# Kernel tuning notes

Measured on AMD Instinct MI355X. Metric: run time of the kernel, lower is better.

The kernel has to match this reference:

```python
import jax, jax.numpy as jnp
import numpy as np

B, N, F_IN, C_OUT = 128, 512, 2, 64
C_IN = F_IN + C_OUT           # 66, concat(input, state) feature dim
MLP_IN = (2 * 3 + 1) * C_IN   # order=2, support_len=3 -> 462


def _gcn(x, supports, W, b):
    """Diffusion conv: x [B,N,F]; for each support a, 2 diffusion orders."""
    outs = [x]
    for a in supports:
        x1 = jnp.einsum('bnf,nm->bmf', x, a)
        x2 = jnp.einsum('bnf,nm->bmf', x1, a)
        outs += [x1, x2]
    h = jnp.concatenate(outs, axis=2)  # [B, N, 7*F]
    return h @ W + b                   # Linear (dropout is eval-mode identity)


def setup_inputs() -> dict:
    key = jax.random.key(0)
    ks = jax.random.split(key, 12)
    return {
        'input': jax.random.normal(ks[0], (B, N, F_IN), dtype=jnp.float32),
        'state': jax.random.normal(ks[1], (B, N, C_OUT), dtype=jnp.float32),
        'A0':    jax.random.uniform(ks[2], (N, N), dtype=jnp.float32),
        'A1':    jax.random.uniform(ks[3], (N, N), dtype=jnp.float32),
        'nv1_1': jax.random.normal(ks[4], (N, 10), dtype=jnp.float32),
        'nv2_1': jax.random.normal(ks[5], (10, N), dtype=jnp.float32),
        'W1':    jax.random.normal(ks[6], (MLP_IN, 2 * C_OUT), dtype=jnp.float32) * 0.02,
        'b1':    jnp.zeros((2 * C_OUT,), dtype=jnp.float32),
        'nv1_2': jax.random.normal(ks[7], (N, 10), dtype=jnp.float32),
        'nv2_2': jax.random.normal(ks[8], (10, N), dtype=jnp.float32),
        'W2':    jax.random.normal(ks[9], (MLP_IN, C_OUT), dtype=jnp.float32) * 0.02,
        'b2':    jnp.zeros((C_OUT,), dtype=jnp.float32),
    }


def reference(input, state, A0, A1, nv1_1, nv2_1, W1, b1, nv1_2, nv2_2, W2, b2):
    c_out = state.shape[-1]
    # gcn_1: adaptive adjacency + diffusion conv, then sigmoid gating split into r,u
    adp1 = jax.nn.softmax(jax.nn.relu(nv1_1 @ nv2_1), axis=1)
    x = jnp.concatenate([input, state], axis=2)
    value = jax.nn.sigmoid(_gcn(x, [A0, A1, adp1], W1, b1))
    r, u = value[..., :c_out], value[..., c_out:]
    # gcn_2: candidate state
    adp2 = jax.nn.softmax(jax.nn.relu(nv1_2 @ nv2_2), axis=1)
    x2 = jnp.concatenate([input, r * state], axis=2)
    c = jnp.tanh(_gcn(x2, [A0, A1, adp2], W2, b2))
    return u * state + (1.0 - u) * c
```

## Files before the change

### kernel.cpp

```cpp
#include <hip/hip_runtime.h>
#include <math.h>

#define NN 512
#define BB 128
#define CIN 66
#define QQ (BB*CIN)
#define AN ((size_t)NN*NN)
#define HB 480
#define KTOT 480

typedef unsigned short ushort_t;
typedef __attribute__((ext_vector_type(8))) short short8;
typedef __attribute__((ext_vector_type(8))) unsigned short us8;
typedef __attribute__((ext_vector_type(4))) float f32x4;
typedef __attribute__((ext_vector_type(4))) unsigned short us4;

__device__ __forceinline__ size_t pidx(int b, int frow, int n) {
    return ((size_t)(b * 30 + (frow >> 4)) << 13) + ((size_t)(n >> 3) << 7)
         + ((frow & 15) << 3) + (n & 7);
}

__device__ __forceinline__ ushort_t f2bf(float f) {
    unsigned u = __float_as_uint(f);
    u += 0x7FFF + ((u >> 16) & 1);
    return (ushort_t)(u >> 16);
}
__device__ __forceinline__ float bf2f(ushort_t h) {
    return __uint_as_float(((unsigned)h) << 16);
}
__device__ __forceinline__ void split_bf(float f, ushort_t& hi, ushort_t& lo) {
    hi = f2bf(f);
    lo = f2bf(f - bf2f(hi));
}
__device__ __forceinline__ void gload_lds16(const void* g, void* l) {
    __builtin_amdgcn_global_load_lds(
        (const __attribute__((address_space(1))) unsigned*)g,
        (__attribute__((address_space(3))) unsigned*)l, 16, 0, 0);
}

__global__ __launch_bounds__(512) void adp_kernel(const float* __restrict__ nv1,
                                                  const float* __restrict__ nv2,
                                                  float* __restrict__ adp) {
    int n = blockIdx.x;
    int m = threadIdx.x;
    float z = 0.f;
#pragma unroll
    for (int k = 0; k < 10; k++) z = fmaf(nv1[n * 10 + k], nv2[k * NN + m], z);
    z = fmaxf(z, 0.f);

    __shared__ float sred[8];
    int wid  = threadIdx.x >> 6;
    int lane = threadIdx.x & 63;

    float v = z;
#pragma unroll
    for (int off = 32; off; off >>= 1) v = fmaxf(v, __shfl_down(v, off, 64));
    if (lane == 0) sred[wid] = v;
    __syncthreads();
    float zmax = sred[0];
#pragma unroll
    for (int i = 1; i < 8; i++) zmax = fmaxf(zmax, sred[i]);

    float e = __expf(z - zmax);
    __syncthreads();
    v = e;
#pragma unroll
    for (int off = 32; off; off >>= 1) v += __shfl_down(v, off, 64);
    if (lane == 0) sred[wid] = v;
    __syncthreads();
    float tot = 0.f;
#pragma unroll
    for (int i = 0; i < 8; i++) tot += sred[i];

    adp[n * NN + m] = e / tot;
}

__global__ __launch_bounds__(256) void asplit_kernel(const float* __restrict__ A0,
                                                     const float* __restrict__ A1,
                                                     const float* __restrict__ P1,
                                                     const float* __restrict__ P2,
                                                     ushort_t* __restrict__ Ahi,
                                                     ushort_t* __restrict__ Alo) {
    __shared__ float t[32][33];
    int s = blockIdx.z;
    const float* src = (s == 0) ? A0 : (s == 1) ? A1 : (s == 2) ? P1 : P2;
    int m0 = blockIdx.x * 32, k0 = blockIdx.y * 32;
    int tx = threadIdx.x & 31, ty = threadIdx.x >> 5;
#pragma unroll
    for (int r = 0; r < 32; r += 8)
        t[ty + r][tx] = src[(size_t)(k0 + ty + r) * NN + m0 + tx];
    __syncthreads();
#pragma unroll
    for (int r = 0; r < 32; r += 8) {
        int m = m0 + ty + r, k = k0 + tx;
        float v = t[tx][ty + r];
        ushort_t h, l; split_bf(v, h, l);
        int mt = m >> 4, l15 = m & 15;
        int kt = k >> 5, quad = (k >> 3) & 3, j = k & 7;
        size_t o = ((((size_t)s * 16 + kt) * 32 + mt) * 64 + quad * 16 + l15) * 8 + j;
        Ahi[o] = h; Alo[o] = l;
    }
}

template <int COUT>
__global__ __launch_bounds__(256) void wtprep_kernel(const float* __restrict__ W,
                                                     ushort_t* __restrict__ Wth,
                                                     ushort_t* __restrict__ Wtl) {
    int j = blockIdx.x;
    for (int k = threadIdx.x; k < KTOT; k += 256) {
        float v = (k < 462) ? W[(size_t)k * COUT + j] : 0.f;
        ushort_t h, l; split_bf(v, h, l);
        Wth[(size_t)j * KTOT + k] = h;
        Wtl[(size_t)j * KTOT + k] = l;
    }
}

__global__ __launch_bounds__(256) void buildx_kernel(const float* __restrict__ inp,
                                                     const float* __restrict__ st,
                                                     ushort_t* __restrict__ Xh,
                                                     ushort_t* __restrict__ Xl) {
    int gid = blockIdx.x * 256 + threadIdx.x;
    int ch  = gid & 63;
    int c   = (gid >> 6) % CIN;
    int b   = gid / (64 * CIN);
    int n0  = ch * 8;
    us8 h8, l8;
#pragma unroll
    for (int r = 0; r < 8; r++) {
        int n = n0 + r;
        float v = (c < 2) ? inp[((size_t)b * NN + n) * 2 + c]
                          : st[((size_t)b * NN + n) * 64 + (c - 2)];
        ushort_t h, l; split_bf(v, h, l);
        h8[r] = h; l8[r] = l;
    }
    size_t o = pidx(b, c, n0);
    *(us8*)&Xh[o] = h8;
    *(us8*)&Xl[o] = l8;
}

__global__ __launch_bounds__(512) void diff_fused(const ushort_t* __restrict__ Aph,
                                                  const ushort_t* __restrict__ Apl,
                                                  ushort_t* Xh, ushort_t* Xl, int s2) {
    const int tid  = threadIdx.x;
    const int lane = tid & 63, w = tid >> 6;
    const int quad = lane >> 4, l15 = lane & 15;
    const int q0 = blockIdx.x * 64;
    const int sz = blockIdx.z;
    const int sup = (sz < 2) ? sz : s2;
    const size_t abase = (size_t)sup * 262144;
    const int mtg0 = w * 4;

    int bq[4], cq[4];
#pragma unroll
    for (int qt = 0; qt < 4; qt++) {
        int q = q0 + qt * 16 + l15;
        bq[qt] = q / 66;
        cq[qt] = q - 66 * bq[qt];
    }

#define DMFMA4(ACC, AH, AL, XH, XL)                                                                \
    {                                                                                              \
        _Pragma("unroll")                                                                          \
        for (int mt = 0; mt < 4; mt++) {                                                           \
            _Pragma("unroll")                                                                      \
            for (int qt = 0; qt < 4; qt++) {                                                       \
                ACC[mt][qt] = __builtin_amdgcn_mfma_f32_16x16x32_bf16(AH[mt], XH[qt], ACC[mt][qt], 0, 0, 0); \
                ACC[mt][qt] = __builtin_amdgcn_mfma_f32_16x16x32_bf16(AH[mt], XL[qt], ACC[mt][qt], 0, 0, 0); \
                ACC[mt][qt] = __builtin_amdgcn_mfma_f32_16x16x32_bf16(AL[mt], XH[qt], ACC[mt][qt], 0, 0, 0); \
                ACC[mt][qt] = __builtin_amdgcn_mfma_f32_16x16x32_bf16(AL[mt], XL[qt], ACC[mt][qt], 0, 0, 0); \
            }                                                                                      \
        }                                                                                          \
    }

    {
        const ushort_t* xph[4];
        const ushort_t* xpl[4];
#pragma unroll
        for (int qt = 0; qt < 4; qt++) {
            int c = cq[qt];
            size_t off = ((size_t)(bq[qt] * 30 + (c >> 4)) << 13) + ((c & 15) << 3)
                       + (size_t)quad * 128;
            xph[qt] = Xh + off;
            xpl[qt] = Xl + off;
        }
        f32x4 acc[4][4] = {};
        for (int kt = 0; kt < 16; kt++) {
            short8 ah[4], al[4], xh4[4], xl4[4];
#pragma unroll
            for (int t = 0; t < 4; t++) {
                size_t fo = abase + ((size_t)kt * 32 + mtg0 + t) * 512 + lane * 8;
                ah[t] = *(const short8*)&Aph[fo];
                al[t] = *(const short8*)&Apl[fo];
            }
#pragma unroll
            for (int qt = 0; qt < 4; qt++) {
                xh4[qt] = *(const short8*)&xph[qt][(size_t)kt * 512];
                xl4[qt] = *(const short8*)&xpl[qt][(size_t)kt * 512];
            }
            DMFMA4(acc, ah, al, xh4, xl4);
        }
        const int rowo = 66 + 132 * sz;
#pragma unroll
        for (int qt = 0; qt < 4; qt++) {
            int frow = rowo + cq[qt];
#pragma unroll
            for (int mt = 0; mt < 4; mt++) {
                int n = w * 64 + mt * 16 + quad * 4;
                us4 h4, l4;
#pragma unroll
                for (int r = 0; r < 4; r++) {
                    ushort_t h, l; split_bf(acc[mt][qt][r], h, l);
                    h4[r] = h; l4[r] = l;
                }
                size_t o = pidx(bq[qt], frow, n);
                *(us4*)&Xh[o] = h4;
                *(us4*)&Xl[o] = l4;
            }
        }
    }
    __syncthreads();

    {
        const int rowi = 66 + 132 * sz;
        const ushort_t* xph[4];
        const ushort_t* xpl[4];
#pragma unroll
        for (int qt = 0; qt < 4; qt++) {
            int frow = rowi + cq[qt];
            size_t off = ((size_t)(bq[qt] * 30 + (frow >> 4)) << 13) + ((frow & 15) << 3)
                       + (size_t)quad * 128;
            xph[qt] = Xh + off;
            xpl[qt] = Xl + off;
        }
        f32x4 acc[4][4] = {};
        for (int kt = 0; kt < 16; kt++) {
            short8 ah[4], al[4], xh4[4], xl4[4];
#pragma unroll
            for (int t = 0; t < 4; t++) {
                size_t fo = abase + ((size_t)kt * 32 + mtg0 + t) * 512 + lane * 8;
                ah[t] = *(const short8*)&Aph[fo];
                al[t] = *(const short8*)&Apl[fo];
            }
#pragma unroll
            for (int qt = 0; qt < 4; qt++) {
                xh4[qt] = *(const short8*)&xph[qt][(size_t)kt * 512];
                xl4[qt] = *(const short8*)&xpl[qt][(size_t)kt * 512];
            }
            DMFMA4(acc, ah, al, xh4, xl4);
        }
        const int rowo = 132 + 132 * sz;
#pragma unroll
        for (int qt = 0; qt < 4; qt++) {
            int frow = rowo + cq[qt];
#pragma unroll
            for (int mt = 0; mt < 4; mt++) {
                int n = w * 64 + mt * 16 + quad * 4;
                us4 h4, l4;
#pragma unroll
                for (int r = 0; r < 4; r++) {
                    ushort_t h, l; split_bf(acc[mt][qt][r], h, l);
                    h4[r] = h; l4[r] = l;
                }
                size_t o = pidx(bq[qt], frow, n);
                *(us4*)&Xh[o] = h4;
                *(us4*)&Xl[o] = l4;
            }
        }
    }
#undef DMFMA4
}

template <int COUT, int LAYER, int BM>
__global__ __launch_bounds__(256) void proj_mfma(const ushort_t* XhC, const ushort_t* XlC,
                                                 const ushort_t* __restrict__ Wth,
                                                 const ushort_t* __restrict__ Wtl,
                                                 const float* __restrict__ bias,
                                                 const float* __restrict__ state,
                                                 float* U,
                                                 ushort_t* Xhw, ushort_t* Xlw,
                                                 float* __restrict__ out) {
    __shared__ ushort_t sAh[BM * 32];
    __shared__ ushort_t sAl[BM * 32];
    __shared__ ushort_t sBh[COUT * 32];
    __shared__ ushort_t sBl[COUT * 32];
    constexpr int PB = COUT / 64;
    const int tid  = threadIdx.x;
    const int lane = tid & 63, w = tid >> 6;
    const int quad = lane >> 4, l15 = lane & 15;
    const int b = blockIdx.y, n0 = blockIdx.x * BM;
    const int wn = (COUT == 128) ? (w & 1) : w;
    const int wj = (COUT == 128) ? (w >> 1) : 0;
    const int kp = tid & 15, n8 = tid >> 4;

    size_t boff[PB]; int lB[PB];
#pragma unroll
    for (int p = 0; p < PB; p++) {
        int cid = p * 256 + tid;
        lB[p]   = cid * 8;
        boff[p] = (size_t)(cid >> 2) * KTOT + (cid & 3) * 8;
    }

    f32x4 acc[4][4] = {};

    for (int k0 = 0; k0 < KTOT; k0 += 32) {
        __syncthreads();
#pragma unroll
        for (int pass = 0; pass < BM / 128; pass++) {
            int np0 = (n8 + pass * 16) * 8;
            int kk  = k0 + 2 * kp;
            size_t o = pidx(b, kk, n0 + np0);
            us8 h0 = *(const us8*)&XhC[o];
            us8 h1 = *(const us8*)&XhC[o + 8];
            us8 l0 = *(const us8*)&XlC[o];
            us8 l1 = *(const us8*)&XlC[o + 8];
            int g = kp >> 2, ko = (2 * kp) & 7;
#pragma unroll
            for (int j2 = 0; j2 < 8; j2++) {
                int n   = np0 + j2;
                int idx = n * 32 + ((g ^ ((n >> 1) & 3)) << 3) + ko;
                *(unsigned*)&sAh[idx] = (unsigned)h0[j2] | ((unsigned)h1[j2] << 16);
                *(unsigned*)&sAl[idx] = (unsigned)l0[j2] | ((unsigned)l1[j2] << 16);
            }
        }
#pragma unroll
        for (int p = 0; p < PB; p++) {
            gload_lds16(Wth + boff[p] + k0, sBh + lB[p]);
            gload_lds16(Wtl + boff[p] + k0, sBl + lB[p]);
        }
        __syncthreads();
        short8 ah[4], al[4], bh[4], bl[4];
#pragma unroll
        for (int t = 0; t < 4; t++) {
            int an  = wn * 64 + t * 16 + l15;
            int ago = (quad ^ ((an >> 1) & 3)) << 3;
            ah[t] = *(const short8*)&sAh[an * 32 + ago];
            al[t] = *(const short8*)&sAl[an * 32 + ago];
            int brow = wj * 64 + t * 16 + l15;
            bh[t] = *(const short8*)&sBh[brow * 32 + quad * 8];
            bl[t] = *(const short8*)&sBl[brow * 32 + quad * 8];
        }
#pragma unroll
        for (int nt = 0; nt < 4; nt++)
#pragma unroll
            for (int jt = 0; jt < 4; jt++) {
                acc[nt][jt] = __builtin_amdgcn_mfma_f32_16x16x32_bf16(ah[nt], bh[jt], acc[nt][jt], 0, 0, 0);
                acc[nt][jt] = __builtin_amdgcn_mfma_f32_16x16x32_bf16(ah[nt], bl[jt], acc[nt][jt], 0, 0, 0);
                acc[nt][jt] = __builtin_amdgcn_mfma_f32_16x16x32_bf16(al[nt], bh[jt], acc[nt][jt], 0, 0, 0);
                acc[nt][jt] = __builtin_amdgcn_mfma_f32_16x16x32_bf16(al[nt], bl[jt], acc[nt][jt], 0, 0, 0);
            }
    }

#pragma unroll
    for (int jt = 0; jt < 4; jt++) {
        int j = wj * 64 + jt * 16 + l15;
        float bj = bias[j];
#pragma unroll
        for (int nt = 0; nt < 4; nt++) {
            int nb = n0 + wn * 64 + nt * 16 + quad * 4;
            f32x4 z = acc[nt][jt];
#pragma unroll
            for (int r = 0; r < 4; r++) z[r] += bj;
            if (LAYER == 1) {
#pragma unroll
                for (int r = 0; r < 4; r++) z[r] = 1.f / (1.f + __expf(-z[r]));
                if (j < 64) {
                    us4 h4, l4;
#pragma unroll
                    for (int r = 0; r < 4; r++) {
                        float x2 = z[r] * state[((size_t)b * NN + nb + r) * 64 + j];
                        ushort_t h, l; split_bf(x2, h, l);
                        h4[r] = h; l4[r] = l;
                    }
                    size_t o = pidx(b, 2 + j, nb);
                    *(us4*)&Xhw[o] = h4;
                    *(us4*)&Xlw[o] = l4;
                } else {
                    *(f32x4*)&U[((size_t)b * 64 + j - 64) * NN + nb] = z;
                }
            } else {
                f32x4 u4 = *(const f32x4*)&U[((size_t)b * 64 + j) * NN + nb];
#pragma unroll
                for (int r = 0; r < 4; r++) {
                    float c = tanhf(z[r]);
                    float s = state[((size_t)b * NN + nb + r) * 64 + j];
                    out[((size_t)b * NN + nb + r) * 64 + j] = u4[r] * s + (1.f - u4[r]) * c;
                }
            }
        }
    }
}

extern "C" void kernel_launch(void* const* d_in, const int* in_sizes, int n_in,
                              void* d_out, int out_size, void* d_ws, size_t ws_size,
                              hipStream_t stream) {
    const float* input = (const float*)d_in[0];
    const float* state = (const float*)d_in[1];
    const float* A0    = (const float*)d_in[2];
    const float* A1    = (const float*)d_in[3];
    const float* nv1_1 = (const float*)d_in[4];
    const float* nv2_1 = (const float*)d_in[5];
    const float* W1    = (const float*)d_in[6];
    const float* b1    = (const float*)d_in[7];
    const float* nv1_2 = (const float*)d_in[8];
    const float* nv2_2 = (const float*)d_in[9];
    const float* W2    = (const float*)d_in[10];
    const float* b2    = (const float*)d_in[11];
    float* out = (float*)d_out;

    char* p = (char*)d_ws;
    auto alloc = [&](size_t bytes) { void* r = (void*)p; p += (bytes + 255) & ~(size_t)255; return r; };
    float*    ADP1 = (float*)alloc(AN * 4);
    float*    ADP2 = (float*)alloc(AN * 4);
    ushort_t* Ahi  = (ushort_t*)alloc(4 * AN * 2);
    ushort_t* Alo  = (ushort_t*)alloc(4 * AN * 2);
    ushort_t* Xh   = (ushort_t*)alloc((size_t)BB * HB * NN * 2);
    ushort_t* Xl   = (ushort_t*)alloc((size_t)BB * HB * NN * 2);
    ushort_t* Wt1h = (ushort_t*)alloc((size_t)128 * KTOT * 2);
    ushort_t* Wt1l = (ushort_t*)alloc((size_t)128 * KTOT * 2);
    ushort_t* Wt2h = (ushort_t*)alloc((size_t)64 * KTOT * 2);
    ushort_t* Wt2l = (ushort_t*)alloc((size_t)64 * KTOT * 2);
    float*    U    = (float*)alloc((size_t)BB * 64 * NN * 4);

    adp_kernel<<<NN, NN, 0, stream>>>(nv1_1, nv2_1, ADP1);
    adp_kernel<<<NN, NN, 0, stream>>>(nv1_2, nv2_2, ADP2);
    asplit_kernel<<<dim3(16, 16, 4), 256, 0, stream>>>(A0, A1, ADP1, ADP2, Ahi, Alo);
    wtprep_kernel<128><<<128, 256, 0, stream>>>(W1, Wt1h, Wt1l);
    wtprep_kernel<64><<<64, 256, 0, stream>>>(W2, Wt2h, Wt2l);
    buildx_kernel<<<BB * CIN * 64 / 256, 256, 0, stream>>>(input, state, Xh, Xl);

    dim3 gf(QQ / 64, 1, 3);
    diff_fused<<<gf, 512, 0, stream>>>(Ahi, Alo, Xh, Xl, 2);
    proj_mfma<128, 1, 128><<<dim3(NN / 128, BB), 256, 0, stream>>>(Xh, Xl, Wt1h, Wt1l, b1, state,
                                                                   U, Xh, Xl, nullptr);
    diff_fused<<<gf, 512, 0, stream>>>(Ahi, Alo, Xh, Xl, 3);
    proj_mfma<64, 2, 256><<<dim3(NN / 256, BB), 256, 0, stream>>>(Xh, Xl, Wt2h, Wt2l, b2, state,
                                                                  U, nullptr, nullptr, out);
}
```

Baseline: 417.9 us.

## Merge prep kernels and keep first diffusion hi-part in LDS for second hop

Merges the two adjacency softmax launches into one grid and fuses the weight-transpose and input-build kernels into a single launch, cutting launch overhead. In diff_fused, the bf16 high part of the first-hop result is also written to a 64KB XOR-swizzled shared buffer. The second hop then reads it from LDS instead of global memory, while the low part still comes from global. The 64KB of LDS per 512-thread block may limit occupancy, and the launch_bounds(512,4) hint may force register spills.

```diff
diff --git a/kernel.cpp b/kernel.cpp
--- a/kernel.cpp
+++ b/kernel.cpp
@@ -38,9 +38,15 @@
         (__attribute__((address_space(3))) unsigned*)l, 16, 0, 0);
 }
 
-__global__ __launch_bounds__(512) void adp_kernel(const float* __restrict__ nv1,
-                                                  const float* __restrict__ nv2,
-                                                  float* __restrict__ adp) {
+__global__ __launch_bounds__(512) void adp_pair_kernel(const float* __restrict__ nv1a,
+                                                       const float* __restrict__ nv2a,
+                                                       const float* __restrict__ nv1b,
+                                                       const float* __restrict__ nv2b,
+                                                       float* __restrict__ adp1,
+                                                       float* __restrict__ adp2) {
+    const float* nv1 = blockIdx.z ? nv1b : nv1a;
+    const float* nv2 = blockIdx.z ? nv2b : nv2a;
+    float* adp       = blockIdx.z ? adp2 : adp1;
     int n = blockIdx.x;
     int m = threadIdx.x;
     float z = 0.f;
@@ -102,45 +108,58 @@
     }
 }
 
-template <int COUT>
-__global__ __launch_bounds__(256) void wtprep_kernel(const float* __restrict__ W,
-                                                     ushort_t* __restrict__ Wth,
-                                                     ushort_t* __restrict__ Wtl) {
-    int j = blockIdx.x;
-    for (int k = threadIdx.x; k < KTOT; k += 256) {
-        float v = (k < 462) ? W[(size_t)k * COUT + j] : 0.f;
-        ushort_t h, l; split_bf(v, h, l);
-        Wth[(size_t)j * KTOT + k] = h;
-        Wtl[(size_t)j * KTOT + k] = l;
-    }
-}
-
-__global__ __launch_bounds__(256) void buildx_kernel(const float* __restrict__ inp,
-                                                     const float* __restrict__ st,
-                                                     ushort_t* __restrict__ Xh,
-                                                     ushort_t* __restrict__ Xl) {
-    int gid = blockIdx.x * 256 + threadIdx.x;
-    int ch  = gid & 63;
-    int c   = (gid >> 6) % CIN;
-    int b   = gid / (64 * CIN);
-    int n0  = ch * 8;
-    us8 h8, l8;
-#pragma unroll
-    for (int r = 0; r < 8; r++) {
-        int n = n0 + r;
-        float v = (c < 2) ? inp[((size_t)b * NN + n) * 2 + c]
-                          : st[((size_t)b * NN + n) * 64 + (c - 2)];
-        ushort_t h, l; split_bf(v, h, l);
-        h8[r] = h; l8[r] = l;
-    }
-    size_t o = pidx(b, c, n0);
-    *(us8*)&Xh[o] = h8;
-    *(us8*)&Xl[o] = l8;
-}
-
-__global__ __launch_bounds__(512) void diff_fused(const ushort_t* __restrict__ Aph,
-                                                  const ushort_t* __restrict__ Apl,
-                                                  ushort_t* Xh, ushort_t* Xl, int s2) {
+__global__ __launch_bounds__(256) void prep_misc_kernel(const float* __restrict__ W1,
+                                                        const float* __restrict__ W2,
+                                                        const float* __restrict__ inp,
+                                                        const float* __restrict__ st,
+                                                        ushort_t* __restrict__ Wt1h,
+                                                        ushort_t* __restrict__ Wt1l,
+                                                        ushort_t* __restrict__ Wt2h,
+                                                        ushort_t* __restrict__ Wt2l,
+                                                        ushort_t* __restrict__ Xh,
+                                                        ushort_t* __restrict__ Xl) {
+    int blk = blockIdx.x;
+    if (blk < 128) {
+        int j = blk;
+        for (int k = threadIdx.x; k < KTOT; k += 256) {
+            float v = (k < 462) ? W1[(size_t)k * 128 + j] : 0.f;
+            ushort_t h, l; split_bf(v, h, l);
+            Wt1h[(size_t)j * KTOT + k] = h;
+            Wt1l[(size_t)j * KTOT + k] = l;
+        }
+    } else if (blk < 192) {
+        int j = blk - 128;
+        for (int k = threadIdx.x; k < KTOT; k += 256) {
+            float v = (k < 462) ? W2[(size_t)k * 64 + j] : 0.f;
+            ushort_t h, l; split_bf(v, h, l);
+            Wt2h[(size_t)j * KTOT + k] = h;
+            Wt2l[(size_t)j * KTOT + k] = l;
+        }
+    } else {
+        int gid = (blk - 192) * 256 + threadIdx.x;
+        int ch  = gid & 63;
+        int c   = (gid >> 6) % CIN;
+        int b   = gid / (64 * CIN);
+        int n0  = ch * 8;
+        us8 h8, l8;
+#pragma unroll
+        for (int r = 0; r < 8; r++) {
+            int n = n0 + r;
+            float v = (c < 2) ? inp[((size_t)b * NN + n) * 2 + c]
+                              : st[((size_t)b * NN + n) * 64 + (c - 2)];
+            ushort_t h, l; split_bf(v, h, l);
+            h8[r] = h; l8[r] = l;
+        }
+        size_t o = pidx(b, c, n0);
+        *(us8*)&Xh[o] = h8;
+        *(us8*)&Xl[o] = l8;
+    }
+}
+
+__global__ __launch_bounds__(512, 4) void diff_fused(const ushort_t* __restrict__ Aph,
+                                                     const ushort_t* __restrict__ Apl,
+                                                     ushort_t* Xh, ushort_t* Xl, int s2) {
+    __shared__ ushort_t sX1h[64 * 512];
     const int tid  = threadIdx.x;
     const int lane = tid & 63, w = tid >> 6;
     const int quad = lane >> 4, l15 = lane & 15;
@@ -150,12 +169,13 @@
     const size_t abase = (size_t)sup * 262144;
     const int mtg0 = w * 4;
 
-    int bq[4], cq[4];
+    int bq[4], cq[4], qloc[4];
 #pragma unroll
     for (int qt = 0; qt < 4; qt++) {
         int q = q0 + qt * 16 + l15;
         bq[qt] = q / 66;
         cq[qt] = q - 66 * bq[qt];
+        qloc[qt] = qt * 16 + l15;
     }
 
 #define DMFMA4(ACC, AH, AL, XH, XL)                                                                \
@@ -215,6 +235,8 @@
                 size_t o = pidx(bq[qt], frow, n);
                 *(us4*)&Xh[o] = h4;
                 *(us4*)&Xl[o] = l4;
+                int chunk = (n >> 3) ^ (qloc[qt] & 7);
+                *(us4*)&sX1h[qloc[qt] * 512 + chunk * 8 + (quad & 1) * 4] = h4;
             }
         }
     }
@@ -222,14 +244,12 @@
 
     {
         const int rowi = 66 + 132 * sz;
-        const ushort_t* xph[4];
         const ushort_t* xpl[4];
 #pragma unroll
         for (int qt = 0; qt < 4; qt++) {
             int frow = rowi + cq[qt];
             size_t off = ((size_t)(bq[qt] * 30 + (frow >> 4)) << 13) + ((frow & 15) << 3)
                        + (size_t)quad * 128;
-            xph[qt] = Xh + off;
             xpl[qt] = Xl + off;
         }
         f32x4 acc[4][4] = {};
@@ -243,7 +263,8 @@
             }
 #pragma unroll
             for (int qt = 0; qt < 4; qt++) {
-                xh4[qt] = *(const short8*)&xph[qt][(size_t)kt * 512];
+                int chunk = (kt * 4 + quad) ^ (qloc[qt] & 7);
+                xh4[qt] = *(const short8*)&sX1h[qloc[qt] * 512 + chunk * 8];
                 xl4[qt] = *(const short8*)&xpl[qt][(size_t)kt * 512];
             }
             DMFMA4(acc, ah, al, xh4, xl4);
@@ -421,12 +442,10 @@
     ushort_t* Wt2l = (ushort_t*)alloc((size_t)64 * KTOT * 2);
     float*    U    = (float*)alloc((size_t)BB * 64 * NN * 4);
 
-    adp_kernel<<<NN, NN, 0, stream>>>(nv1_1, nv2_1, ADP1);
-    adp_kernel<<<NN, NN, 0, stream>>>(nv1_2, nv2_2, ADP2);
+    adp_pair_kernel<<<dim3(NN, 1, 2), NN, 0, stream>>>(nv1_1, nv2_1, nv1_2, nv2_2, ADP1, ADP2);
+    prep_misc_kernel<<<192 + BB * CIN * 64 / 256, 256, 0, stream>>>(W1, W2, input, state,
+                                                                    Wt1h, Wt1l, Wt2h, Wt2l, Xh, Xl);
     asplit_kernel<<<dim3(16, 16, 4), 256, 0, stream>>>(A0, A1, ADP1, ADP2, Ahi, Alo);
-    wtprep_kernel<128><<<128, 256, 0, stream>>>(W1, Wt1h, Wt1l);
-    wtprep_kernel<64><<<64, 256, 0, stream>>>(W2, Wt2h, Wt2l);
-    buildx_kernel<<<BB * CIN * 64 / 256, 256, 0, stream>>>(input, state, Xh, Xl);
 
     dim3 gf(QQ / 64, 1, 3);
     diff_fused<<<gf, 512, 0, stream>>>(Ahi, Alo, Xh, Xl, 2);
```

Result: slower. 438.7 us (+5.0%).
